# Performance work log

Measured on AMD Instinct MI355X. Metric: run time of the kernel, lower is better.

Reference implementation:

```python
import jax, jax.numpy as jnp
import numpy as np

RADIUS = 0.2
K = 32       # nsample
S = 1024     # npoint
BN_EPS = 1e-5


def fps(xyz, s):
    # xyz: [B, N, 3] -> indices [B, s] (farthest point sampling, start at index 0)
    B, N, _ = xyz.shape

    def step(carry, _):
        dist, last = carry                                  # [B,N], [B]
        lp = jnp.take_along_axis(xyz, last[:, None, None], axis=1)  # [B,1,3]
        d = jnp.sum((xyz - lp) ** 2, axis=-1)               # [B,N]
        dist = jnp.minimum(dist, d)
        nxt = jnp.argmax(dist, axis=-1).astype(jnp.int32)
        return (dist, nxt), last

    init = (jnp.full((B, N), jnp.inf, xyz.dtype), jnp.zeros((B,), jnp.int32))
    _, idxs = jax.lax.scan(step, init, None, length=s)      # [s, B]
    return idxs.T                                           # [B, s]


def query_ball(new_xyz, xyz, radius, k):
    # new_xyz: [B,S,3], xyz: [B,N,3] -> first k in-ball indices [B,S,k]
    B, N, _ = xyz.shape
    d2 = jnp.sum((new_xyz[:, :, None, :] - xyz[:, None, :, :]) ** 2, axis=-1)  # [B,S,N]
    cand = jnp.where(d2 <= radius * radius, jnp.arange(N, dtype=jnp.int32)[None, None, :], N)
    idx = jnp.sort(cand, axis=-1)[..., :k]                  # first-k by index, pytorch3d order
    first = idx[..., :1]
    idx = jnp.where(idx == N, first, idx)                   # replicate first valid index
    return jnp.minimum(idx, N - 1)


def gather_pts(pts, idx):
    # pts: [B,N,C], idx: [B,S,K] -> [B,S,K,C]
    B, N, C = pts.shape
    _, s, k = idx.shape
    g = jnp.take_along_axis(pts, idx.reshape(B, s * k, 1), axis=1)
    return g.reshape(B, s, k, C)


def conv_bn_relu(x, W, b, g, be):
    # x: [B,S,K,Cin], W: [Cout,Cin] (1x1 conv), training-mode BatchNorm over (B,S,K)
    y = jnp.einsum('bskc,oc->bsko', x, W) + b
    mu = jnp.mean(y, axis=(0, 1, 2))
    var = jnp.var(y, axis=(0, 1, 2))
    y = (y - mu) * jax.lax.rsqrt(var + BN_EPS) * g + be
    return jax.nn.relu(y)


def setup_inputs() -> dict:
    key = jax.random.key(0)
    ks = jax.random.split(key, 8)
    B, N, D = 8, 8192, 64
    inp = {
        'xyz': jax.random.uniform(ks[0], (B, 3, N), dtype=jnp.float32),
        'points': jax.random.normal(ks[1], (B, D, N), dtype=jnp.float32),
    }
    dims = [(64, 67), (64, 64), (128, 64)]
    for i, (o, c) in enumerate(dims):
        inp[f'W{i}'] = jax.random.normal(ks[2 + i], (o, c), dtype=jnp.float32) * 0.05
        inp[f'b{i}'] = jnp.zeros((o,), jnp.float32)
        inp[f'g{i}'] = jnp.ones((o,), jnp.float32)
        inp[f'be{i}'] = jnp.zeros((o,), jnp.float32)
    return inp


def reference(xyz, points, W0, b0, g0, be0, W1, b1, g1, be1, W2, b2, g2, be2):
    # xyz: [B,3,N], points: [B,D,N]
    xyz_n = jnp.transpose(xyz, (0, 2, 1))                   # [B,N,3]
    pts_n = jnp.transpose(points, (0, 2, 1))                # [B,N,D]
    idx = fps(xyz_n, S)                                     # [B,S]
    new_xyz = jnp.take_along_axis(xyz_n, idx[..., None], axis=1)  # [B,S,3]
    gidx = query_ball(new_xyz, xyz_n, RADIUS, K)            # [B,S,K]
    gxyz = (gather_pts(xyz_n, gidx) - new_xyz[:, :, None, :]) / RADIUS  # [B,S,K,3]
    gpts = gather_pts(pts_n, gidx)                          # [B,S,K,D]
    feat = jnp.concatenate([gpts, gxyz], axis=-1)           # [B,S,K,D+3]
    feat = conv_bn_relu(feat, W0, b0, g0, be0)
    feat = conv_bn_relu(feat, W1, b1, g1, be1)
    feat = conv_bn_relu(feat, W2, b2, g2, be2)
    new_points = jnp.max(feat, axis=2)                      # [B,S,Cout]
    return (jnp.transpose(new_xyz, (0, 2, 1)), jnp.transpose(new_points, (0, 2, 1)))
```

## Files before the change

### kernel.cpp

```cpp
#include <hip/hip_runtime.h>

#define BB 8
#define NN 8192
#define SS 1024
#define KK 32
#define NPIX (BB*SS*KK)
#define R2C 0.04f
#define EPS 1e-5f

#define FT 1024
#define FW (FT/64)
#define PPT (NN/FT)
#define NCELL 4096
#define TBLK 64

typedef float v2f __attribute__((ext_vector_type(2)));

#define OFF_IDX      0u
#define OFF_NEWXYZ   (OFF_IDX + BB*SS*4)
#define OFF_GIDX     (OFF_NEWXYZ + BB*SS*3*4)
#define OFF_XYZN     (OFF_GIDX + BB*SS*KK*4)
#define OFF_PTSN     (OFF_XYZN + BB*NN*3*4)
#define OFF_Y0       (OFF_PTSN + BB*NN*64*4)
#define OFF_Y1       (OFF_Y0 + NPIX*64*2)
#define OFF_MAXMIN   (OFF_Y1 + NPIX*64*2)
#define OFF_P0       (OFF_MAXMIN + BB*SS*128*2*4)
#define OFF_P1       (OFF_P0 + 1024*128*4)
#define OFF_P2       (OFF_P1 + 1024*128*4)
#define OFF_SC       (OFF_P2 + 1024*256*4)

__device__ __forceinline__ unsigned short f2bf(float x){
    unsigned u = __float_as_uint(x);
    unsigned r = (u + 0x7FFFu + ((u >> 16) & 1u)) >> 16;
    return (unsigned short)r;
}
__device__ __forceinline__ float bf2f(unsigned h){
    return __uint_as_float(h << 16);
}
__device__ __forceinline__ float sqdist3(float dx, float dy, float dz){
    return __fadd_rn(__fadd_rn(__fmul_rn(dx,dx), __fmul_rn(dy,dy)), __fmul_rn(dz,dz));
}
__device__ __forceinline__ int spread4(int v){
    return (v&1) | ((v&2)<<2) | ((v&4)<<4) | ((v&8)<<6);
}

template<int CTRL>
__device__ __forceinline__ unsigned long long dpp_max_step(unsigned long long k){
    int lo = (int)(unsigned)k;
    int hi = (int)(unsigned)(k >> 32);
    int olo = __builtin_amdgcn_update_dpp(0, lo, CTRL, 0xf, 0xf, true);
    int ohi = __builtin_amdgcn_update_dpp(0, hi, CTRL, 0xf, 0xf, true);
    unsigned long long o = ((unsigned long long)(unsigned)ohi << 32) | (unsigned)olo;
    return (o > k) ? o : k;
}
__device__ __forceinline__ unsigned long long wave_max_u64(unsigned long long k){
    k = dpp_max_step<0x111>(k); k = dpp_max_step<0x112>(k);
    k = dpp_max_step<0x114>(k); k = dpp_max_step<0x118>(k);
    k = dpp_max_step<0x142>(k); k = dpp_max_step<0x143>(k);
    return k;
}

template<int CTRL>
__device__ __forceinline__ float dpp_sum_step(float v){
    int o = __builtin_amdgcn_update_dpp(0, __float_as_int(v), CTRL, 0xf, 0xf, true);
    return v + __int_as_float(o);
}
__device__ __forceinline__ float wave_sum_f32(float v){
    v = dpp_sum_step<0x111>(v); v = dpp_sum_step<0x112>(v);
    v = dpp_sum_step<0x114>(v); v = dpp_sum_step<0x118>(v);
    v = dpp_sum_step<0x142>(v); v = dpp_sum_step<0x143>(v);
    return v;
}
template<int CTRL>
__device__ __forceinline__ float dpp_max_stepf(float v){
    int o = __builtin_amdgcn_update_dpp(__float_as_int(v), __float_as_int(v), CTRL, 0xf, 0xf, false);
    return fmaxf(v, __int_as_float(o));
}
template<int CTRL>
__device__ __forceinline__ float dpp_min_stepf(float v){
    int o = __builtin_amdgcn_update_dpp(__float_as_int(v), __float_as_int(v), CTRL, 0xf, 0xf, false);
    return fminf(v, __int_as_float(o));
}
__device__ __forceinline__ float grp32_max(float v){
    v = dpp_max_stepf<0x111>(v); v = dpp_max_stepf<0x112>(v);
    v = dpp_max_stepf<0x114>(v); v = dpp_max_stepf<0x118>(v);
    v = dpp_max_stepf<0x142>(v);
    return v;
}
__device__ __forceinline__ float grp32_min(float v){
    v = dpp_min_stepf<0x111>(v); v = dpp_min_stepf<0x112>(v);
    v = dpp_min_stepf<0x114>(v); v = dpp_min_stepf<0x118>(v);
    v = dpp_min_stepf<0x142>(v);
    return v;
}

__global__ __launch_bounds__(FT) void fps_kernel(const float* __restrict__ xyz,
                                                 const float* __restrict__ pts,
                                                 float* __restrict__ newxyz,
                                                 float* __restrict__ out,
                                                 float* __restrict__ xyz_n,
                                                 float* __restrict__ pts_n){
    __shared__ float sxyz[NN * 3];
    __shared__ int   si[NN];
    __shared__ int   hist[NCELL];
    __shared__ int   waveTot[FW];
    __shared__ unsigned long long cells[SS];
    int tid = threadIdx.x;

    if (blockIdx.x >= 8){
        int gid = (blockIdx.x - 8) * FT + tid;
        int b = gid >> 13, i = gid & (NN - 1);
        const float* xb = xyz + (size_t)b * 3 * NN;
        float x = xb[i], y = xb[NN + i], z = xb[2 * NN + i];
        float* xd = xyz_n + ((size_t)b * NN + i) * 3;
        xd[0] = x; xd[1] = y; xd[2] = z;
        const float* pb = pts + (size_t)b * 64 * NN + i;
        float4* pd = (float4*)(pts_n + ((size_t)b * NN + i) * 64);
#pragma unroll
        for (int q = 0; q < 16; ++q){
            float4 v;
            v.x = pb[(q*4+0)*NN]; v.y = pb[(q*4+1)*NN];
            v.z = pb[(q*4+2)*NN]; v.w = pb[(q*4+3)*NN];
            pd[q] = v;
        }
        return;
    }

    int b = blockIdx.x;
    int wave = tid >> 6, lane = tid & 63;
    const float* xb = xyz + (size_t)b * 3 * NN;

    int cell[PPT];
#pragma unroll
    for (int j = 0; j < PPT; ++j){
        int i = tid + j * FT;
        float x = xb[i], y = xb[NN + i], z = xb[2*NN + i];
        sxyz[i*3]   = x; sxyz[i*3+1] = y; sxyz[i*3+2] = z;
        int cx = min(15, max(0, (int)(x * 16.f)));
        int cy = min(15, max(0, (int)(y * 16.f)));
        int cz = min(15, max(0, (int)(z * 16.f)));
        cell[j] = spread4(cx) | (spread4(cy) << 1) | (spread4(cz) << 2);
    }
#pragma unroll
    for (int k = 0; k < NCELL/FT; ++k) hist[tid * (NCELL/FT) + k] = 0;
    cells[tid] = 0ull;
    __syncthreads();
#pragma unroll
    for (int j = 0; j < PPT; ++j) atomicAdd(&hist[cell[j]], 1);
    __syncthreads();
    {
        int base0 = tid * (NCELL/FT);
        int sum4 = 0;
#pragma unroll
        for (int k = 0; k < NCELL/FT; ++k) sum4 += hist[base0 + k];
        int s = sum4;
#pragma unroll
        for (int m = 1; m < 64; m <<= 1){
            int v = __shfl_up(s, m);
            if (lane >= m) s += v;
        }
        if (lane == 63) waveTot[wave] = s;
        __syncthreads();
        int wbase = 0;
#pragma unroll
        for (int w2 = 0; w2 < FW; ++w2) if (w2 < wave) wbase += waveTot[w2];
        int run = wbase + s - sum4;
#pragma unroll
        for (int k = 0; k < NCELL/FT; ++k){
            int h = hist[base0 + k];
            hist[base0 + k] = run;
            run += h;
        }
    }
    __syncthreads();
#pragma unroll
    for (int j = 0; j < PPT; ++j){
        int pos = atomicAdd(&hist[cell[j]], 1);
        si[pos] = tid + j * FT;
    }
    __syncthreads();
    v2f px[PPT/2], py[PPT/2], pz[PPT/2];
    float dist[PPT];
    int oi[PPT];
    float bxmin =  1e30f, bxmax = -1e30f;
    float bymin =  1e30f, bymax = -1e30f;
    float bzmin =  1e30f, bzmax = -1e30f;
#pragma unroll
    for (int j = 0; j < PPT; ++j){
        int g = si[tid * PPT + j];
        oi[j] = g;
        float x = sxyz[g*3], y = sxyz[g*3+1], z = sxyz[g*3+2];
        px[j>>1][j&1] = x; py[j>>1][j&1] = y; pz[j>>1][j&1] = z;
        bxmin = fminf(bxmin, x); bxmax = fmaxf(bxmax, x);
        bymin = fminf(bymin, y); bymax = fmaxf(bymax, y);
        bzmin = fminf(bzmin, z); bzmax = fmaxf(bzmax, z);
        dist[j] = __int_as_float(0x7f800000);
    }
    __syncthreads();

    unsigned long long mykey = 0ull;
    unsigned long long lane63cache = 0ull;
    float tmax = __int_as_float(0x7f800000);
    int w = 0;
    for (int t = 0; t < SS; ++t){
        if (tid == 0) hist[t] = w;
        int w3 = w * 3;
        float lx = sxyz[w3], ly = sxyz[w3+1], lz = sxyz[w3+2];
        float cdx = __fsub_rn(lx, fminf(fmaxf(lx, bxmin), bxmax));
        float cdy = __fsub_rn(ly, fminf(fmaxf(ly, bymin), bymax));
        float cdz = __fsub_rn(lz, fminf(fmaxf(lz, bzmin), bzmax));
        float d_bb = sqdist3(cdx, cdy, cdz);
        bool active = d_bb < tmax;
        unsigned long long bal = __ballot(active);
        if (active){
            {
#pragma clang fp contract(off)
                v2f lx2 = {lx, lx}, ly2 = {ly, ly}, lz2 = {lz, lz};
#pragma unroll
                for (int p = 0; p < PPT/2; ++p){
                    v2f dx = px[p] - lx2;
                    v2f dy = py[p] - ly2;
                    v2f dz = pz[p] - lz2;
                    v2f d  = ((dx*dx) + (dy*dy)) + (dz*dz);
                    dist[2*p]   = fminf(dist[2*p],   d[0]);
                    dist[2*p+1] = fminf(dist[2*p+1], d[1]);
                }
            }
            float m0 = fmaxf(dist[0], dist[1]);
            float m1 = fmaxf(dist[2], dist[3]);
            float m2 = fmaxf(dist[4], dist[5]);
            float m3 = fmaxf(dist[6], dist[7]);
            m0 = fmaxf(m0, m1); m2 = fmaxf(m2, m3);
            float maxd = fmaxf(m0, m2);
            int bo = 0x7fffffff;
#pragma unroll
            for (int j = 0; j < PPT; ++j)
                if (dist[j] == maxd) bo = min(bo, oi[j]);
            mykey = ((unsigned long long)__float_as_uint(maxd) << 32)
                  | (unsigned)(~bo);
            tmax = maxd;
        }
        if (bal){
            unsigned long long k = wave_max_u64(mykey);
            if (lane == 63) lane63cache = k;
        }
        if (lane == 63) atomicMax(&cells[t], lane63cache);
        __syncthreads();
        unsigned long long km = cells[t];
        w = (int)(~(unsigned)km);
    }
    __syncthreads();
    for (int t2 = tid; t2 < SS; t2 += FT){
        int hw = hist[t2] * 3;
        float x = sxyz[hw], y = sxyz[hw+1], z = sxyz[hw+2];
        out[(size_t)b * 3 * SS + t2]          = x;
        out[(size_t)b * 3 * SS + SS + t2]     = y;
        out[(size_t)b * 3 * SS + 2*SS + t2]   = z;
        float* nw = newxyz + ((size_t)b * SS + t2) * 3;
        nw[0] = x; nw[1] = y; nw[2] = z;
    }
}

__global__ __launch_bounds__(256) void qb_kernel(const float* __restrict__ xyz,
                                                 const float* __restrict__ newxyz,
                                                 int* __restrict__ gidx){
    int wid = (blockIdx.x * 256 + threadIdx.x) >> 6;
    int lane = threadIdx.x & 63;
    int b = wid >> 10;
    const float* nw = newxyz + (size_t)wid * 3;
    float cx = nw[0], cy = nw[1], cz = nw[2];
    const float* xb = xyz + (size_t)b * 3 * NN;
    int total = 0, firstIdx = -1;
    int* gout = gidx + (size_t)wid * KK;
    for (int base = 0; base < NN; base += 64){
        int i = base + lane;
        float dx = __fsub_rn(cx, xb[i]);
        float dy = __fsub_rn(cy, xb[NN + i]);
        float dz = __fsub_rn(cz, xb[2*NN + i]);
        float d2 = sqdist3(dx, dy, dz);
        bool in = (d2 <= R2C);
        unsigned long long m = __ballot(in);
        int pos = total + __popcll(m & ((1ull << lane) - 1ull));
        if (in && pos < KK) gout[pos] = i;
        if (firstIdx < 0 && m) firstIdx = base + (__ffsll((unsigned long long)m) - 1);
        total += __popcll(m);
        if (total >= KK) break;
    }
    if (total < KK){
        int f = (total > 0) ? firstIdx : (NN - 1);
        for (int p = total + lane; p < KK; p += 64) gout[p] = f;
    }
}

__global__ __launch_bounds__(256) void l0_kernel(const float* __restrict__ pts_n,
                                                 const float* __restrict__ xyz_n,
                                                 const float* __restrict__ newxyz,
                                                 const int* __restrict__ gidx,
                                                 const float* __restrict__ W0,
                                                 const float* __restrict__ b0,
                                                 uint4* __restrict__ y0,
                                                 float* __restrict__ part0){
    __shared__ float lsum[4][64][2];
    int tid = threadIdx.x;
    int pixel = blockIdx.x * 256 + tid;
    int sample = pixel >> 5;
    int b = sample >> 10;
    int gi = gidx[pixel];
    int wave = tid >> 6, lane = tid & 63;

    float ff[67];
    const float4* prow = (const float4*)(pts_n + ((size_t)b * NN + gi) * 64);
#pragma unroll
    for (int q = 0; q < 16; ++q){
        float4 v = prow[q];
        ff[q*4] = v.x; ff[q*4+1] = v.y; ff[q*4+2] = v.z; ff[q*4+3] = v.w;
    }
    const float* pr = xyz_n + ((size_t)b * NN + gi) * 3;
    const float* nw = newxyz + (size_t)sample * 3;
    ff[64] = __fsub_rn(pr[0], nw[0]) / 0.2f;
    ff[65] = __fsub_rn(pr[1], nw[1]) / 0.2f;
    ff[66] = __fsub_rn(pr[2], nw[2]) / 0.2f;

    for (int oc = 0; oc < 8; ++oc){
        float acc[8];
#pragma unroll
        for (int j = 0; j < 8; ++j) acc[j] = b0[oc*8+j];
#pragma unroll
        for (int c = 0; c < 67; ++c){
            float fe = ff[c];
#pragma unroll
            for (int j = 0; j < 8; ++j) acc[j] += fe * W0[(oc*8+j)*67 + c];
        }
        uint4 pk;
        unsigned us[8];
#pragma unroll
        for (int j = 0; j < 8; ++j){
            float v = acc[j];
            float s1 = wave_sum_f32(v);
            float s2 = wave_sum_f32(v * v);
            if (lane == 63){ lsum[wave][oc*8+j][0] = s1; lsum[wave][oc*8+j][1] = s2; }
            us[j] = f2bf(v);
        }
        pk.x = us[0] | (us[1] << 16);
        pk.y = us[2] | (us[3] << 16);
        pk.z = us[4] | (us[5] << 16);
        pk.w = us[6] | (us[7] << 16);
        y0[(size_t)pixel * 8 + oc] = pk;
    }
    __syncthreads();
    if (tid < 128){
        float s = lsum[0][tid>>1][tid&1] + lsum[1][tid>>1][tid&1]
                + lsum[2][tid>>1][tid&1] + lsum[3][tid>>1][tid&1];
        part0[(size_t)blockIdx.x * 128 + tid] = s;
    }
}

__global__ __launch_bounds__(256) void l1_kernel(const uint4* __restrict__ y0,
                                                 const float* __restrict__ scale0,
                                                 const float* __restrict__ shift0,
                                                 const float* __restrict__ W1,
                                                 const float* __restrict__ b1,
                                                 uint4* __restrict__ y1,
                                                 float* __restrict__ part1){
    __shared__ float lsum[4][64][2];
    int tid = threadIdx.x;
    int pixel = blockIdx.x * 256 + tid;
    int wave = tid >> 6, lane = tid & 63;

    float x[64];
#pragma unroll
    for (int q = 0; q < 8; ++q){
        uint4 v = y0[(size_t)pixel * 8 + q];
        unsigned w[4] = {v.x, v.y, v.z, v.w};
#pragma unroll
        for (int r = 0; r < 4; ++r){
            int c = q*8 + r*2;
            x[c]   = fmaxf(bf2f(w[r] & 0xFFFFu) * scale0[c]   + shift0[c],   0.f);
            x[c+1] = fmaxf(bf2f(w[r] >> 16)     * scale0[c+1] + shift0[c+1], 0.f);
        }
    }
    for (int oc = 0; oc < 8; ++oc){
        float acc[8];
#pragma unroll
        for (int j = 0; j < 8; ++j) acc[j] = b1[oc*8+j];
#pragma unroll
        for (int c = 0; c < 64; ++c){
            float fe = x[c];
#pragma unroll
            for (int j = 0; j < 8; ++j) acc[j] += fe * W1[(oc*8+j)*64 + c];
        }
        uint4 pk;
        unsigned us[8];
#pragma unroll
        for (int j = 0; j < 8; ++j){
            float v = acc[j];
            float s1 = wave_sum_f32(v);
            float s2 = wave_sum_f32(v * v);
            if (lane == 63){ lsum[wave][oc*8+j][0] = s1; lsum[wave][oc*8+j][1] = s2; }
            us[j] = f2bf(v);
        }
        pk.x = us[0] | (us[1] << 16);
        pk.y = us[2] | (us[3] << 16);
        pk.z = us[4] | (us[5] << 16);
        pk.w = us[6] | (us[7] << 16);
        y1[(size_t)pixel * 8 + oc] = pk;
    }
    __syncthreads();
    if (tid < 128){
        float s = lsum[0][tid>>1][tid&1] + lsum[1][tid>>1][tid&1]
                + lsum[2][tid>>1][tid&1] + lsum[3][tid>>1][tid&1];
        part1[(size_t)blockIdx.x * 128 + tid] = s;
    }
}

__global__ __launch_bounds__(256) void l2_kernel(const uint4* __restrict__ y1,
                                                 const float* __restrict__ scale1,
                                                 const float* __restrict__ shift1,
                                                 const float* __restrict__ W2,
                                                 const float* __restrict__ b2,
                                                 float* __restrict__ maxmin,
                                                 float* __restrict__ part2){
    __shared__ float lsum[4][128][2];
    int tid = threadIdx.x;
    int pixel = blockIdx.x * 256 + tid;
    int sample = pixel >> 5;
    int wave = tid >> 6, lane = tid & 63;

    float x[64];
#pragma unroll
    for (int q = 0; q < 8; ++q){
        uint4 v = y1[(size_t)pixel * 8 + q];
        unsigned w[4] = {v.x, v.y, v.z, v.w};
#pragma unroll
        for (int r = 0; r < 4; ++r){
            int c = q*8 + r*2;
            x[c]   = fmaxf(bf2f(w[r] & 0xFFFFu) * scale1[c]   + shift1[c],   0.f);
            x[c+1] = fmaxf(bf2f(w[r] >> 16)     * scale1[c+1] + shift1[c+1], 0.f);
        }
    }
    for (int oc = 0; oc < 16; ++oc){
        float acc[8];
#pragma unroll
        for (int j = 0; j < 8; ++j) acc[j] = b2[oc*8+j];
#pragma unroll
        for (int c = 0; c < 64; ++c){
            float fe = x[c];
#pragma unroll
            for (int j = 0; j < 8; ++j) acc[j] += fe * W2[(oc*8+j)*64 + c];
        }
#pragma unroll
        for (int j = 0; j < 8; ++j){
            float v = acc[j];
            int ch = oc*8 + j;
            float mx = grp32_max(v);
            float mn = grp32_min(v);
            float s1 = wave_sum_f32(v);
            float s2 = wave_sum_f32(v * v);
            if (lane == 63){ lsum[wave][ch][0] = s1; lsum[wave][ch][1] = s2; }
            if ((tid & 31) == 31){
                float* mm = maxmin + ((size_t)sample * 128 + ch) * 2;
                mm[0] = mx; mm[1] = mn;
            }
        }
    }
    __syncthreads();
    {
        float s = lsum[0][tid>>1][tid&1] + lsum[1][tid>>1][tid&1]
                + lsum[2][tid>>1][tid&1] + lsum[3][tid>>1][tid&1];
        part2[(size_t)blockIdx.x * 256 + tid] = s;
    }
}

__global__ __launch_bounds__(1024) void fin_kernel(const float* __restrict__ part, int O,
                           const float* __restrict__ g, const float* __restrict__ be,
                           float* __restrict__ scale, float* __restrict__ shift){
    __shared__ float4 ls[1024];
    int tid = threadIdx.x;
    int M = 2 * O;
    int V = M >> 2;
    int NC = 1024 / V;
    int q = tid & (V - 1);
    int c = tid / V;
    int per = 1024 / NC;
    const float4* p4 = (const float4*)part;
    float4 s = {0.f, 0.f, 0.f, 0.f};
    for (int r = 0; r < per; ++r){
        int blk = c * per + r;
        float4 v = p4[(size_t)blk * V + q];
        s.x += v.x; s.y += v.y; s.z += v.z; s.w += v.w;
    }
    ls[c * V + q] = s;
    __syncthreads();
    if (tid < V){
        float4 t4 = ls[tid];
        for (int c2 = 1; c2 < NC; ++c2){
            float4 v = ls[c2 * V + tid];
            t4.x += v.x; t4.y += v.y; t4.z += v.z; t4.w += v.w;
        }
        float inv = 1.0f / (float)NPIX;
        int ch0 = 2 * tid, ch1 = 2 * tid + 1;
        float mu0 = t4.x * inv;
        float var0 = t4.y * inv - mu0 * mu0;
        float sc0 = (1.0f / sqrtf(var0 + EPS)) * g[ch0];
        scale[ch0] = sc0; shift[ch0] = be[ch0] - mu0 * sc0;
        float mu1 = t4.z * inv;
        float var1 = t4.w * inv - mu1 * mu1;
        float sc1 = (1.0f / sqrtf(var1 + EPS)) * g[ch1];
        scale[ch1] = sc1; shift[ch1] = be[ch1] - mu1 * sc1;
    }
}

__global__ __launch_bounds__(256) void out_kernel(const float* __restrict__ maxmin,
                                                  const float* __restrict__ scale2,
                                                  const float* __restrict__ shift2,
                                                  float* __restrict__ out){
    int gid = blockIdx.x * 256 + threadIdx.x;
    int s = gid & 1023;
    int o = (gid >> 10) & 127;
    int b = gid >> 17;
    int sample = b * 1024 + s;
    float2 mm = ((const float2*)maxmin)[(size_t)sample * 128 + o];
    float sc = scale2[o], sh = shift2[o];
    float v = (sc >= 0.f) ? mm.x : mm.y;
    out[gid] = fmaxf(v * sc + sh, 0.f);
}

extern "C" void kernel_launch(void* const* d_in, const int* in_sizes, int n_in,
                              void* d_out, int out_size, void* d_ws, size_t ws_size,
                              hipStream_t stream) {
    const float* xyz = (const float*)d_in[0];
    const float* pts = (const float*)d_in[1];
    const float* W0 = (const float*)d_in[2];
    const float* b0 = (const float*)d_in[3];
    const float* g0 = (const float*)d_in[4];
    const float* be0 = (const float*)d_in[5];
    const float* W1 = (const float*)d_in[6];
    const float* b1 = (const float*)d_in[7];
    const float* g1 = (const float*)d_in[8];
    const float* be1 = (const float*)d_in[9];
    const float* W2 = (const float*)d_in[10];
    const float* b2 = (const float*)d_in[11];
    const float* g2 = (const float*)d_in[12];
    const float* be2 = (const float*)d_in[13];

    char* ws = (char*)d_ws;
    float* newxyz = (float*)(ws + OFF_NEWXYZ);
    int*   gidx   = (int*)(ws + OFF_GIDX);
    float* xyz_n  = (float*)(ws + OFF_XYZN);
    float* pts_n  = (float*)(ws + OFF_PTSN);
    uint4* y0     = (uint4*)(ws + OFF_Y0);
    uint4* y1     = (uint4*)(ws + OFF_Y1);
    float* maxmin = (float*)(ws + OFF_MAXMIN);
    float* part0  = (float*)(ws + OFF_P0);
    float* part1  = (float*)(ws + OFF_P1);
    float* part2  = (float*)(ws + OFF_P2);
    float* sc     = (float*)(ws + OFF_SC);
    float* scale0 = sc,        *shift0 = sc + 64;
    float* scale1 = sc + 128,  *shift1 = sc + 192;
    float* scale2 = sc + 256,  *shift2 = sc + 384;

    float* out = (float*)d_out;
    float* out_np = out + BB * 3 * SS;

    hipLaunchKernelGGL(fps_kernel, dim3(8 + TBLK), dim3(FT), 0, stream,
                       xyz, pts, newxyz, out, xyz_n, pts_n);
    hipLaunchKernelGGL(qb_kernel, dim3(2048), dim3(256), 0, stream, xyz, newxyz, gidx);
    hipLaunchKernelGGL(l0_kernel, dim3(1024), dim3(256), 0, stream,
                       pts_n, xyz_n, newxyz, gidx, W0, b0, y0, part0);
    hipLaunchKernelGGL(fin_kernel, dim3(1), dim3(1024), 0, stream, part0, 64, g0, be0, scale0, shift0);
    hipLaunchKernelGGL(l1_kernel, dim3(1024), dim3(256), 0, stream,
                       y0, scale0, shift0, W1, b1, y1, part1);
    hipLaunchKernelGGL(fin_kernel, dim3(1), dim3(1024), 0, stream, part1, 64, g1, be1, scale1, shift1);
    hipLaunchKernelGGL(l2_kernel, dim3(1024), dim3(256), 0, stream,
                       y1, scale1, shift1, W2, b2, maxmin, part2);
    hipLaunchKernelGGL(fin_kernel, dim3(1), dim3(1024), 0, stream, part2, 128, g2, be2, scale2, shift2);
    hipLaunchKernelGGL(out_kernel, dim3(4096), dim3(256), 0, stream, maxmin, scale2, shift2, out_np);
}
```

Baseline: 1.238 ms.

## Fuse MLP layers into cooperative kernel with grid syncs; simplify FPS wave argmax

The three conv+BN layers, their statistics-finalisation kernels and the output kernel are replaced by one cooperative kernel of 256 blocks of 1024 threads. It uses grid.sync between the BN stages, keeps layer-0 activations in registers and no longer writes y0 to memory. The FPS loop replaces its 64-bit DPP wave max with a float max followed by a 32-bit min over tied indices. The fused kernel carries 64+ float arrays per thread at 1024 threads per block, which risks register spills or the cooperative launch failing; in that case the original multi-kernel path runs as a fallback.

Result: slower. 1.338 ms (+8.1%).

```diff
diff --git a/kernel.cpp b/kernel.cpp
--- a/kernel.cpp
+++ b/kernel.cpp
@@ -1,4 +1,7 @@
 #include <hip/hip_runtime.h>
+#include <hip/hip_cooperative_groups.h>
+
+namespace cg = cooperative_groups;
 
 #define BB 8
 #define NN 8192
@@ -45,21 +48,20 @@
 }
 
 template<int CTRL>
-__device__ __forceinline__ unsigned long long dpp_max_step(unsigned long long k){
-    int lo = (int)(unsigned)k;
-    int hi = (int)(unsigned)(k >> 32);
-    int olo = __builtin_amdgcn_update_dpp(0, lo, CTRL, 0xf, 0xf, true);
-    int ohi = __builtin_amdgcn_update_dpp(0, hi, CTRL, 0xf, 0xf, true);
-    unsigned long long o = ((unsigned long long)(unsigned)ohi << 32) | (unsigned)olo;
-    return (o > k) ? o : k;
-}
-__device__ __forceinline__ unsigned long long wave_max_u64(unsigned long long k){
-    k = dpp_max_step<0x111>(k); k = dpp_max_step<0x112>(k);
-    k = dpp_max_step<0x114>(k); k = dpp_max_step<0x118>(k);
-    k = dpp_max_step<0x142>(k); k = dpp_max_step<0x143>(k);
-    return k;
-}
-
+__device__ __forceinline__ float dppf_max(float v){
+    int o = __builtin_amdgcn_update_dpp(__float_as_int(v), __float_as_int(v), CTRL, 0xf, 0xf, false);
+    return fmaxf(v, __int_as_float(o));
+}
+template<int CTRL>
+__device__ __forceinline__ float dppf_min(float v){
+    int o = __builtin_amdgcn_update_dpp(__float_as_int(v), __float_as_int(v), CTRL, 0xf, 0xf, false);
+    return fminf(v, __int_as_float(o));
+}
+template<int CTRL>
+__device__ __forceinline__ unsigned dppu_min(unsigned v){
+    unsigned o = (unsigned)__builtin_amdgcn_update_dpp((int)v, (int)v, CTRL, 0xf, 0xf, false);
+    return min(v, o);
+}
 template<int CTRL>
 __device__ __forceinline__ float dpp_sum_step(float v){
     int o = __builtin_amdgcn_update_dpp(0, __float_as_int(v), CTRL, 0xf, 0xf, true);
@@ -71,26 +73,28 @@
     v = dpp_sum_step<0x142>(v); v = dpp_sum_step<0x143>(v);
     return v;
 }
-template<int CTRL>
-__device__ __forceinline__ float dpp_max_stepf(float v){
-    int o = __builtin_amdgcn_update_dpp(__float_as_int(v), __float_as_int(v), CTRL, 0xf, 0xf, false);
-    return fmaxf(v, __int_as_float(o));
-}
-template<int CTRL>
-__device__ __forceinline__ float dpp_min_stepf(float v){
-    int o = __builtin_amdgcn_update_dpp(__float_as_int(v), __float_as_int(v), CTRL, 0xf, 0xf, false);
-    return fminf(v, __int_as_float(o));
-}
 __device__ __forceinline__ float grp32_max(float v){
-    v = dpp_max_stepf<0x111>(v); v = dpp_max_stepf<0x112>(v);
-    v = dpp_max_stepf<0x114>(v); v = dpp_max_stepf<0x118>(v);
-    v = dpp_max_stepf<0x142>(v);
+    v = dppf_max<0x111>(v); v = dppf_max<0x112>(v);
+    v = dppf_max<0x114>(v); v = dppf_max<0x118>(v);
+    v = dppf_max<0x142>(v);
     return v;
 }
 __device__ __forceinline__ float grp32_min(float v){
-    v = dpp_min_stepf<0x111>(v); v = dpp_min_stepf<0x112>(v);
-    v = dpp_min_stepf<0x114>(v); v = dpp_min_stepf<0x118>(v);
-    v = dpp_min_stepf<0x142>(v);
+    v = dppf_min<0x111>(v); v = dppf_min<0x112>(v);
+    v = dppf_min<0x114>(v); v = dppf_min<0x118>(v);
+    v = dppf_min<0x142>(v);
+    return v;
+}
+__device__ __forceinline__ float wave_max_f32(float v){
+    v = dppf_max<0x111>(v); v = dppf_max<0x112>(v);
+    v = dppf_max<0x114>(v); v = dppf_max<0x118>(v);
+    v = dppf_max<0x142>(v); v = dppf_max<0x143>(v);
+    return v;
+}
+__device__ __forceinline__ unsigned wave_min_u32(unsigned v){
+    v = dppu_min<0x111>(v); v = dppu_min<0x112>(v);
+    v = dppu_min<0x114>(v); v = dppu_min<0x118>(v);
+    v = dppu_min<0x142>(v); v = dppu_min<0x143>(v);
     return v;
 }
 
@@ -198,9 +202,9 @@
     }
     __syncthreads();
 
-    unsigned long long mykey = 0ull;
-    unsigned long long lane63cache = 0ull;
     float tmax = __int_as_float(0x7f800000);
+    int   bidx = 0;
+    unsigned long long wkey = 0ull;
     int w = 0;
     for (int t = 0; t < SS; ++t){
         if (tid == 0) hist[t] = w;
@@ -212,42 +216,43 @@
         float d_bb = sqdist3(cdx, cdy, cdz);
         bool active = d_bb < tmax;
         unsigned long long bal = __ballot(active);
-        if (active){
-            {
+        if (bal){
+            if (active){
+                {
 #pragma clang fp contract(off)
-                v2f lx2 = {lx, lx}, ly2 = {ly, ly}, lz2 = {lz, lz};
-#pragma unroll
-                for (int p = 0; p < PPT/2; ++p){
-                    v2f dx = px[p] - lx2;
-                    v2f dy = py[p] - ly2;
-                    v2f dz = pz[p] - lz2;
-                    v2f d  = ((dx*dx) + (dy*dy)) + (dz*dz);
-                    dist[2*p]   = fminf(dist[2*p],   d[0]);
-                    dist[2*p+1] = fminf(dist[2*p+1], d[1]);
+                    v2f lx2 = {lx, lx}, ly2 = {ly, ly}, lz2 = {lz, lz};
+#pragma unroll
+                    for (int p = 0; p < PPT/2; ++p){
+                        v2f dx = px[p] - lx2;
+                        v2f dy = py[p] - ly2;
+                        v2f dz = pz[p] - lz2;
+                        v2f d  = ((dx*dx) + (dy*dy)) + (dz*dz);
+                        dist[2*p]   = fminf(dist[2*p],   d[0]);
+                        dist[2*p+1] = fminf(dist[2*p+1], d[1]);
+                    }
                 }
+                float m0 = fmaxf(dist[0], dist[1]);
+                float m1 = fmaxf(dist[2], dist[3]);
+                float m2 = fmaxf(dist[4], dist[5]);
+                float m3 = fmaxf(dist[6], dist[7]);
+                m0 = fmaxf(m0, m1); m2 = fmaxf(m2, m3);
+                float maxd = fmaxf(m0, m2);
+                int bo = 0x7fffffff;
+#pragma unroll
+                for (int j = 0; j < PPT; ++j)
+                    if (dist[j] == maxd) bo = min(bo, oi[j]);
+                tmax = maxd; bidx = bo;
             }
-            float m0 = fmaxf(dist[0], dist[1]);
-            float m1 = fmaxf(dist[2], dist[3]);
-            float m2 = fmaxf(dist[4], dist[5]);
-            float m3 = fmaxf(dist[6], dist[7]);
-            m0 = fmaxf(m0, m1); m2 = fmaxf(m2, m3);
-            float maxd = fmaxf(m0, m2);
-            int bo = 0x7fffffff;
-#pragma unroll
-            for (int j = 0; j < PPT; ++j)
-                if (dist[j] == maxd) bo = min(bo, oi[j]);
-            mykey = ((unsigned long long)__float_as_uint(maxd) << 32)
-                  | (unsigned)(~bo);
-            tmax = maxd;
-        }
-        if (bal){
-            unsigned long long k = wave_max_u64(mykey);
-            if (lane == 63) lane63cache = k;
-        }
-        if (lane == 63) atomicMax(&cells[t], lane63cache);
+            float m = wave_max_f32(tmax);
+            float sm = __int_as_float(__builtin_amdgcn_readlane(__float_as_int(m), 63));
+            unsigned cand = (tmax == sm) ? (unsigned)bidx : 0xFFFFFFFFu;
+            cand = wave_min_u32(cand);
+            unsigned sidx = (unsigned)__builtin_amdgcn_readlane((int)cand, 63);
+            wkey = ((unsigned long long)__float_as_uint(sm) << 32) | (unsigned)(~sidx);
+        }
+        if (lane == 63) atomicMax(&cells[t], wkey);
         __syncthreads();
-        unsigned long long km = cells[t];
-        w = (int)(~(unsigned)km);
+        w = (int)(~(unsigned)cells[t]);
     }
     __syncthreads();
     for (int t2 = tid; t2 < SS; t2 += FT){
@@ -292,6 +297,211 @@
     }
 }
 
+__device__ void fin_block0(const float* __restrict__ part, int O,
+                           const float* __restrict__ g, const float* __restrict__ be,
+                           float* __restrict__ scale, float* __restrict__ shift,
+                           float* fs){
+    int tid = threadIdx.x;
+    int M = 2 * O;
+    int C = 1024 / M;
+    int m = tid & (M - 1);
+    int chunk = tid / M;
+    int per = 256 / C;
+    float s = 0.f;
+    for (int r = 0; r < per; ++r)
+        s += part[(size_t)(chunk * per + r) * M + m];
+    fs[tid] = s;
+    __syncthreads();
+    float t = 0.f;
+    if (tid < M){
+        for (int c2 = 0; c2 < C; ++c2) t += fs[c2 * M + tid];
+    }
+    __syncthreads();
+    if (tid < M) fs[tid] = t;
+    __syncthreads();
+    if (tid < O){
+        float s1 = fs[2*tid], s2 = fs[2*tid+1];
+        float inv = 1.0f / (float)NPIX;
+        float mu = s1 * inv;
+        float var = s2 * inv - mu * mu;
+        float sc = (1.0f / sqrtf(var + EPS)) * g[tid];
+        scale[tid] = sc;
+        shift[tid] = be[tid] - mu * sc;
+    }
+    __syncthreads();
+}
+
+__global__ __launch_bounds__(1024) void mlp_kernel(
+        const float* __restrict__ pts_n, const float* __restrict__ xyz_n,
+        const float* __restrict__ newxyz, const int* __restrict__ gidx,
+        const float* __restrict__ W0, const float* __restrict__ b0,
+        const float* __restrict__ g0, const float* __restrict__ be0,
+        const float* __restrict__ W1, const float* __restrict__ b1,
+        const float* __restrict__ g1, const float* __restrict__ be1,
+        const float* __restrict__ W2, const float* __restrict__ b2,
+        const float* __restrict__ g2, const float* __restrict__ be2,
+        uint4* __restrict__ y1buf, float* __restrict__ maxmin,
+        float* __restrict__ part0, float* __restrict__ part1, float* __restrict__ part2,
+        float* __restrict__ scale0, float* __restrict__ shift0,
+        float* __restrict__ scale1, float* __restrict__ shift1,
+        float* __restrict__ scale2, float* __restrict__ shift2,
+        float* __restrict__ out_np){
+    cg::grid_group grid = cg::this_grid();
+    __shared__ float lsum[16][128][2];
+    __shared__ float fs[1024];
+    int tid = threadIdx.x;
+    int pixel = blockIdx.x * 1024 + tid;
+    int sample = pixel >> 5;
+    int b = sample >> 10;
+    int wave = tid >> 6, lane = tid & 63;
+
+    float y0f[64];
+#pragma unroll
+    for (int j = 0; j < 64; ++j) y0f[j] = b0[j];
+    {
+        int gi = gidx[pixel];
+        const float4* prow = (const float4*)(pts_n + ((size_t)b * NN + gi) * 64);
+#pragma unroll
+        for (int q = 0; q < 16; ++q){
+            float4 v = prow[q];
+            int c = q * 4;
+#pragma unroll
+            for (int j = 0; j < 64; ++j){
+                y0f[j] += v.x * W0[j*67 + c]   + v.y * W0[j*67 + c+1]
+                        + v.z * W0[j*67 + c+2] + v.w * W0[j*67 + c+3];
+            }
+        }
+        const float* pr = xyz_n + ((size_t)b * NN + gi) * 3;
+        const float* nw = newxyz + (size_t)sample * 3;
+#pragma unroll
+        for (int k = 0; k < 3; ++k){
+            float fe = __fsub_rn(pr[k], nw[k]) / 0.2f;
+#pragma unroll
+            for (int j = 0; j < 64; ++j) y0f[j] += fe * W0[j*67 + 64 + k];
+        }
+    }
+#pragma unroll
+    for (int j = 0; j < 64; ++j){
+        float v = y0f[j];
+        float s1 = wave_sum_f32(v);
+        float s2 = wave_sum_f32(v * v);
+        if (lane == 63){ lsum[wave][j][0] = s1; lsum[wave][j][1] = s2; }
+    }
+    __syncthreads();
+    if (tid < 128){
+        float s = 0.f;
+#pragma unroll
+        for (int w2 = 0; w2 < 16; ++w2) s += lsum[w2][tid>>1][tid&1];
+        part0[(size_t)blockIdx.x * 128 + tid] = s;
+    }
+    grid.sync();
+    if (blockIdx.x == 0) fin_block0(part0, 64, g0, be0, scale0, shift0, fs);
+    grid.sync();
+
+#pragma unroll
+    for (int c = 0; c < 64; ++c)
+        y0f[c] = fmaxf(y0f[c] * scale0[c] + shift0[c], 0.f);
+    for (int oc = 0; oc < 8; ++oc){
+        float acc[8];
+#pragma unroll
+        for (int j = 0; j < 8; ++j) acc[j] = b1[oc*8+j];
+#pragma unroll
+        for (int c = 0; c < 64; ++c){
+            float fe = y0f[c];
+#pragma unroll
+            for (int j = 0; j < 8; ++j) acc[j] += fe * W1[(oc*8+j)*64 + c];
+        }
+        uint4 pk;
+        unsigned us[8];
+#pragma unroll
+        for (int j = 0; j < 8; ++j){
+            float v = acc[j];
+            float s1 = wave_sum_f32(v);
+            float s2 = wave_sum_f32(v * v);
+            if (lane == 63){ lsum[wave][oc*8+j][0] = s1; lsum[wave][oc*8+j][1] = s2; }
+            us[j] = f2bf(v);
+        }
+        pk.x = us[0] | (us[1] << 16);
+        pk.y = us[2] | (us[3] << 16);
+        pk.z = us[4] | (us[5] << 16);
+        pk.w = us[6] | (us[7] << 16);
+        y1buf[(size_t)pixel * 8 + oc] = pk;
+    }
+    __syncthreads();
+    if (tid < 128){
+        float s = 0.f;
+#pragma unroll
+        for (int w2 = 0; w2 < 16; ++w2) s += lsum[w2][tid>>1][tid&1];
+        part1[(size_t)blockIdx.x * 128 + tid] = s;
+    }
+    grid.sync();
+    if (blockIdx.x == 0) fin_block0(part1, 64, g1, be1, scale1, shift1, fs);
+    grid.sync();
+
+    {
+        float x[64];
+#pragma unroll
+        for (int q = 0; q < 8; ++q){
+            uint4 v = y1buf[(size_t)pixel * 8 + q];
+            unsigned wv[4] = {v.x, v.y, v.z, v.w};
+#pragma unroll
+            for (int r = 0; r < 4; ++r){
+                int c = q*8 + r*2;
+                x[c]   = fmaxf(bf2f(wv[r] & 0xFFFFu) * scale1[c]   + shift1[c],   0.f);
+                x[c+1] = fmaxf(bf2f(wv[r] >> 16)     * scale1[c+1] + shift1[c+1], 0.f);
+            }
+        }
+        for (int oc = 0; oc < 16; ++oc){
+            float acc[8];
+#pragma unroll
+            for (int j = 0; j < 8; ++j) acc[j] = b2[oc*8+j];
+#pragma unroll
+            for (int c = 0; c < 64; ++c){
+                float fe = x[c];
+#pragma unroll
+                for (int j = 0; j < 8; ++j) acc[j] += fe * W2[(oc*8+j)*64 + c];
+            }
+#pragma unroll
+            for (int j = 0; j < 8; ++j){
+                float v = acc[j];
+                int ch = oc*8 + j;
+                float mx = grp32_max(v);
+                float mn = grp32_min(v);
+                float s1 = wave_sum_f32(v);
+                float s2 = wave_sum_f32(v * v);
+                if (lane == 63){ lsum[wave][ch][0] = s1; lsum[wave][ch][1] = s2; }
+                if ((tid & 31) == 31){
+                    float* mm = maxmin + ((size_t)sample * 128 + ch) * 2;
+                    mm[0] = mx; mm[1] = mn;
+                }
+            }
+        }
+        __syncthreads();
+        if (tid < 256){
+            float s = 0.f;
+#pragma unroll
+            for (int w2 = 0; w2 < 16; ++w2) s += lsum[w2][tid>>1][tid&1];
+            part2[(size_t)blockIdx.x * 256 + tid] = s;
+        }
+    }
+    grid.sync();
+    if (blockIdx.x == 0) fin_block0(part2, 128, g2, be2, scale2, shift2, fs);
+    grid.sync();
+
+#pragma unroll
+    for (int k = 0; k < 4; ++k){
+        int gid = blockIdx.x * 4096 + k * 1024 + tid;
+        int s = gid & 1023;
+        int o = (gid >> 10) & 127;
+        int bb = gid >> 17;
+        int smp = bb * 1024 + s;
+        float2 mm = ((const float2*)maxmin)[(size_t)smp * 128 + o];
+        float sc = scale2[o], sh = shift2[o];
+        float v = (sc >= 0.f) ? mm.x : mm.y;
+        out_np[gid] = fmaxf(v * sc + sh, 0.f);
+    }
+}
+
 __global__ __launch_bounds__(256) void l0_kernel(const float* __restrict__ pts_n,
                                                  const float* __restrict__ xyz_n,
                                                  const float* __restrict__ newxyz,
@@ -565,14 +775,32 @@
     hipLaunchKernelGGL(fps_kernel, dim3(8 + TBLK), dim3(FT), 0, stream,
                        xyz, pts, newxyz, out, xyz_n, pts_n);
     hipLaunchKernelGGL(qb_kernel, dim3(2048), dim3(256), 0, stream, xyz, newxyz, gidx);
-    hipLaunchKernelGGL(l0_kernel, dim3(1024), dim3(256), 0, stream,
-                       pts_n, xyz_n, newxyz, gidx, W0, b0, y0, part0);
-    hipLaunchKernelGGL(fin_kernel, dim3(1), dim3(1024), 0, stream, part0, 64, g0, be0, scale0, shift0);
-    hipLaunchKernelGGL(l1_kernel, dim3(1024), dim3(256), 0, stream,
-                       y0, scale0, shift0, W1, b1, y1, part1);
-    hipLaunchKernelGGL(fin_kernel, dim3(1), dim3(1024), 0, stream, part1, 64, g1, be1, scale1, shift1);
-    hipLaunchKernelGGL(l2_kernel, dim3(1024), dim3(256), 0, stream,
-                       y1, scale1, shift1, W2, b2, maxmin, part2);
-    hipLaunchKernelGGL(fin_kernel, dim3(1), dim3(1024), 0, stream, part2, 128, g2, be2, scale2, shift2);
-    hipLaunchKernelGGL(out_kernel, dim3(4096), dim3(256), 0, stream, maxmin, scale2, shift2, out_np);
-}
+
+    void* args[] = {
+        (void*)&pts_n, (void*)&xyz_n, (void*)&newxyz, (void*)&gidx,
+        (void*)&W0, (void*)&b0, (void*)&g0, (void*)&be0,
+        (void*)&W1, (void*)&b1, (void*)&g1, (void*)&be1,
+        (void*)&W2, (void*)&b2, (void*)&g2, (void*)&be2,
+        (void*)&y1, (void*)&maxmin,
+        (void*)&part0, (void*)&part1, (void*)&part2,
+        (void*)&scale0, (void*)&shift0,
+        (void*)&scale1, (void*)&shift1,
+        (void*)&scale2, (void*)&shift2,
+        (void*)&out_np
+    };
+    hipError_t cerr = hipLaunchCooperativeKernel((void*)mlp_kernel, dim3(256), dim3(1024),
+                                                 args, 0, stream);
+    if (cerr != hipSuccess){
+        (void)hipGetLastError();
+        hipLaunchKernelGGL(l0_kernel, dim3(1024), dim3(256), 0, stream,
+                           pts_n, xyz_n, newxyz, gidx, W0, b0, y0, part0);
+        hipLaunchKernelGGL(fin_kernel, dim3(1), dim3(1024), 0, stream, part0, 64, g0, be0, scale0, shift0);
+        hipLaunchKernelGGL(l1_kernel, dim3(1024), dim3(256), 0, stream,
+                           y0, scale0, shift0, W1, b1, y1, part1);
+        hipLaunchKernelGGL(fin_kernel, dim3(1), dim3(1024), 0, stream, part1, 64, g1, be1, scale1, shift1);
+        hipLaunchKernelGGL(l2_kernel, dim3(1024), dim3(256), 0, stream,
+                           y1, scale1, shift1, W2, b2, maxmin, part2);
+        hipLaunchKernelGGL(fin_kernel, dim3(1), dim3(1024), 0, stream, part2, 128, g2, be2, scale2, shift2);
+        hipLaunchKernelGGL(out_kernel, dim3(4096), dim3(256), 0, stream, maxmin, scale2, shift2, out_np);
+    }
+}
```
